# Optimization experiments

Measured on AMD Instinct MI355X. Metric: run time of the kernel, lower is better.

The kernel has to match this reference:

```python
import jax, jax.numpy as jnp
import numpy as np

N, E, G = 65536, 524288, 2048
HID, NLVL = 256, 50
SIG_BEGIN, SIG_END = 10.0, 0.01


def _silu(v):
    return v * jax.nn.sigmoid(v)


def _seg_sum(v, seg, num):
    return jax.ops.segment_sum(v, seg, num_segments=num)


def _seg_mean(v, seg, num):
    s = _seg_sum(v, seg, num)
    cnt = _seg_sum(jnp.ones((v.shape[0], 1), v.dtype), seg, num)
    return s / jnp.maximum(cnt, 1.0)


def setup_inputs() -> dict:
    key = jax.random.key(0)
    ks = jax.random.split(key, 24)
    sc = 1.0 / np.sqrt(HID)
    inp = {
        "x": jax.random.normal(ks[0], (N, HID), jnp.float32),
        "pos": jax.random.normal(ks[1], (N, 3), jnp.float32),
        "noise": jax.random.normal(ks[2], (N, 3), jnp.float32),
        "node2graph": jnp.sort(jax.random.randint(ks[3], (N,), 0, G)),
        "edge_index": jax.random.randint(ks[4], (2, E), 0, N),
        "noise_level": jax.random.randint(ks[5], (G,), 0, NLVL),
        # stand-in rep_model weights
        "W_node": jax.random.normal(ks[6], (HID, HID), jnp.float32) * sc,
        "W_msg": jax.random.normal(ks[7], (HID, HID), jnp.float32) * sc,
        "w_gate": jax.random.normal(ks[8], (HID, 1), jnp.float32) * sc,
        # node_dec
        "Wd1": jax.random.normal(ks[9], (HID, HID), jnp.float32) * sc,
        "bd1": jnp.zeros((HID,), jnp.float32),
        "Wd2": jax.random.normal(ks[10], (HID, HID), jnp.float32) * sc,
        "bd2": jnp.zeros((HID,), jnp.float32),
        # graph_dec
        "Wg1": jax.random.normal(ks[11], (HID, HID), jnp.float32) * sc,
        "bg1": jnp.zeros((HID,), jnp.float32),
        "Wg2": jax.random.normal(ks[12], (HID, 1), jnp.float32) * sc,
        "bg2": jnp.zeros((1,), jnp.float32),
        # noise_pred
        "Wp1": jax.random.normal(ks[13], (2 * HID, HID), jnp.float32) * sc,
        "bp1": jnp.zeros((HID,), jnp.float32),
        "Wp2": jax.random.normal(ks[14], (HID, NLVL), jnp.float32) * sc,
        "bp2": jnp.zeros((NLVL,), jnp.float32),
    }
    return inp


def _rep_model(x, pos, edge_index, W_node, W_msg, w_gate):
    # minimal one-layer equivariant stand-in for the external GNN rep_model
    row, col = edge_index[0], edge_index[1]
    msg = x[row] @ W_msg                                   # [E,H]
    agg = _seg_sum(msg, col, x.shape[0])                   # [N,H]
    xl = _silu(x @ W_node + agg)
    coef = _silu(msg @ w_gate)                             # [E,1]
    posl = pos + _seg_sum((pos[row] - pos[col]) * coef, col, x.shape[0])
    return xl, posl


def _fit_pos(pos_p, pos, n2g, num_g):
    # Kabsch alignment with batched 3x3 SVD (torch.svd: H = U S V^T, R = V U^T)
    center = _seg_mean(pos, n2g, num_g)                    # [G,3]
    pcenter = _seg_mean(pos_p, n2g, num_g)
    pos_c = pos - center[n2g]
    ppc = pos_p - pcenter[n2g]
    # H[g,i,j] = sum_n ppc[n,i]*pos_c[n,j] (matches repeat/repeat_interleave layout)
    Hmat = _seg_sum(jnp.einsum("ni,nj->nij", ppc, pos_c).reshape(-1, 9), n2g, num_g).reshape(-1, 3, 3)
    U, S, Vh = jnp.linalg.svd(Hmat)
    V = jnp.swapaxes(Vh, -1, -2)
    R = V @ jnp.swapaxes(U, -1, -2)                        # [G,3,3]
    t = center - jnp.einsum("gij,gj->gi", R, pcenter)
    return jnp.einsum("nij,nj->ni", R[n2g], pos_p) + t[n2g]


def reference(x, pos, noise, node2graph, edge_index, noise_level,
              W_node, W_msg, w_gate, Wd1, bd1, Wd2, bd2,
              Wg1, bg1, Wg2, bg2, Wp1, bp1, Wp2, bp2):
    num_g = noise_level.shape[0]
    sigmas = jnp.exp(jnp.linspace(np.log(SIG_BEGIN), np.log(SIG_END), NLVL)).astype(x.dtype)
    used_sigmas = sigmas[noise_level][node2graph][:, None]  # [N,1]

    # perturb (kabsch) + target, both no_grad in the original
    pos_p = jax.lax.stop_gradient(_fit_pos(pos + noise * used_sigmas, pos, node2graph, num_g))
    target = jax.lax.stop_gradient((pos - pos_p) / used_sigmas)

    def energy_rep(pin):
        xl, posl = _rep_model(x, pin, edge_index, W_node, W_msg, w_gate)
        xl = _silu(xl @ Wd1 + bd1) @ Wd2 + bd2             # node_dec
        xg = _seg_sum(xl, node2graph, num_g)               # scatter_add -> graph rep
        e = (_silu(xg @ Wg1 + bg1) @ Wg2 + bg2)[:, 0]      # graph_dec
        return e, xg, posl

    _, xg_noise, pred_pos = energy_rep(pos_p)
    pred_noise = (pred_pos - pos_p) / used_sigmas          # pred_mode == 'force'
    loss_den = _seg_sum(jnp.sum((pred_noise - target) ** 2, axis=-1), node2graph, num_g)

    _, xg_ori, _ = energy_rep(pos)
    graph_rep = jnp.concatenate([xg_ori, xg_noise], axis=1)
    logits = _silu(graph_rep @ Wp1 + bp1) @ Wp2 + bp2      # [G,NLVL]
    ce = jax.scipy.special.logsumexp(logits, axis=-1) - jnp.take_along_axis(
        logits, noise_level[:, None], axis=1)[:, 0]
    return jnp.stack([loss_den.mean(), ce.mean()])
```

## Files before the change

### kernel.cpp

```cpp
#include <hip/hip_runtime.h>
#include <math.h>

#define NN 65536
#define NE 524288
#define NG 2048
#define HD 256
#define NL 50

typedef unsigned short u16;
typedef unsigned char u8;
typedef __attribute__((ext_vector_type(8))) short short8;
typedef __attribute__((ext_vector_type(4))) float f32x4;
typedef __attribute__((ext_vector_type(4))) unsigned short us4;

__device__ __forceinline__ float bf2f(u16 h){
  union{unsigned int u; float f;} v; v.u = ((unsigned int)h)<<16; return v.f;
}
__device__ __forceinline__ u16 f2bf(float f){
  union{float f; unsigned int u;} v; v.f=f;
  return (u16)((v.u + 0x7FFFu + ((v.u>>16)&1u))>>16);
}
__device__ __forceinline__ float silu_f(float v){ return v/(1.0f+__expf(-v)); }
__device__ __forceinline__ u8 f2e4m3(float v){
  return (u8)__builtin_amdgcn_cvt_pk_fp8_f32(v, v, 0, false);
}
__device__ __forceinline__ float4 e4m3x4(unsigned w){
  float4 r;
  r.x = __builtin_amdgcn_cvt_f32_fp8(w, 0);
  r.y = __builtin_amdgcn_cvt_f32_fp8(w, 1);
  r.z = __builtin_amdgcn_cvt_f32_fp8(w, 2);
  r.w = __builtin_amdgcn_cvt_f32_fp8(w, 3);
  return r;
}

#define WRED(v) { v += __shfl_xor(v,1); v += __shfl_xor(v,2); v += __shfl_xor(v,4); \
                  v += __shfl_xor(v,8); v += __shfl_xor(v,16); v += __shfl_xor(v,32); }

__global__ void k_wmg(const float* __restrict__ Wm, const float* __restrict__ wgate,
                      float* __restrict__ wmg){
  int k = threadIdx.x;
  float s=0.f;
  for(int j=0;j<256;j++) s += Wm[k*256+j]*wgate[j];
  wmg[k]=s;
}

__global__ void k_front(const int* __restrict__ n2g,
                        const float* __restrict__ x, const int* __restrict__ ei,
                        const float* __restrict__ Wn, const float* __restrict__ Wm,
                        const float* __restrict__ Wd1, const float* __restrict__ Wd2,
                        const float* __restrict__ Wp1, const float* __restrict__ Wp2,
                        int* __restrict__ gstart,
                        u8* __restrict__ wn8, u8* __restrict__ wm8, u8* __restrict__ wd18,
                        u16* __restrict__ wd2b, u16* __restrict__ wpeb,
                        u16* __restrict__ wp2b, const float* __restrict__ wmg,
                        u8* __restrict__ xb8, float* __restrict__ cf,
                        int* __restrict__ cnt_e){
  int b = blockIdx.x, t = threadIdx.x;
  if(b < 257){
    int i = b*256 + t;
    if(i>NN) return;
    int cur  = (i<NN)? n2g[i] : NG;
    int prev = (i==0)? -1 : n2g[i-1];
    for(int g=prev+1; g<=cur; ++g) gstart[g]=i;
  } else if(b < 1601){
    int bb = b - 257;
    if(bb < 768){
      int m = bb>>8;
      int idx = (bb&255)*256 + t;
      int k = idx>>8, n = idx&255;
      const float* W = (m==0)? Wn : (m==1)? Wm : Wd1;
      u8* O = (m==0)? wn8 : (m==1)? wm8 : wd18;
      unsigned a = (unsigned)(n*256+k);
      O[a ^ ((unsigned)(n&15)<<3)] = f2e4m3(W[k*256+n]);
    } else if(bb < 1024){
      int idx = (bb-768)*256 + t; int k=idx>>8, n=idx&255;
      wd2b[n*256+k] = f2bf(Wd2[k*256+n]);
    } else if(bb < 1280){
      int idx = (bb-1024)*256 + t; int k=idx>>8, n=idx&255;
      wpeb[n*256+k] = f2bf(Wp1[k*256+n] + Wp1[(k+256)*256+n]);
    } else {
      int idx = (bb-1280)*256 + t; int k=idx&255, n=idx>>8;
      wp2b[n*256+k] = (n<NL)? f2bf(Wp2[k*NL+n]) : (u16)0;
    }
  } else if(b < 17985){
    int wave = t>>6, lane = t&63;
    int i = (b-1601)*4 + wave;
    float4 a = ((const float4*)(x + (size_t)i*256))[lane];
    float4 bb = ((const float4*)wmg)[lane];
    float s = a.x*bb.x + a.y*bb.y + a.z*bb.z + a.w*bb.w;
    unsigned w = __builtin_amdgcn_cvt_pk_fp8_f32(a.x, a.y, 0, false);
    w = __builtin_amdgcn_cvt_pk_fp8_f32(a.z, a.w, w, true);
    *(unsigned*)(xb8 + (size_t)i*256 + lane*4) = w;
    #pragma unroll
    for(int o=32;o;o>>=1) s += __shfl_down(s,o);
    if(lane==0) cf[i]=silu_f(s);
  } else {
    int e = (b-17985)*256 + t;
    if(e<NE) atomicAdd(&cnt_e[ei[NE+e]],1);
  }
}

__global__ __launch_bounds__(256) void k_mid(const float* __restrict__ pos,
        const float* __restrict__ noise, const int* __restrict__ gstart,
        const int* __restrict__ nl, float* __restrict__ sigg,
        float* __restrict__ posp, float* __restrict__ target,
        const int* __restrict__ cnt_e, int* __restrict__ start,
        int* __restrict__ bsum){
  int b = blockIdx.x, t = threadIdx.x;
  if(b >= 512){
    __shared__ int sh[256];
    int bb = b-512, i = bb*256+t;
    int v = cnt_e[i]; sh[t]=v; __syncthreads();
    #pragma unroll
    for(int o=1;o<256;o<<=1){
      int u = (t>=o)? sh[t-o]:0; __syncthreads(); sh[t]+=u; __syncthreads();
    }
    start[i] = sh[t]-v;
    if(t==255) bsum[bb]=sh[255];
    return;
  }
  int wid = (b<<2) + (t>>6);
  int lane = t & 63;
  int s0 = gstart[wid], s1 = gstart[wid+1];
  const double L0 =  2.3025850929940456840;
  const double L1 = -4.6051701859880913680;
  float sg = (float)exp(L0 + (double)nl[wid]*(L1-L0)/49.0);
  if(lane==0) sigg[wid]=sg;

  float sx=0,sy=0,sz=0, tx=0,ty=0,tz=0;
  for(int i=s0+lane;i<s1;i+=64){
    float px=pos[3*i],py=pos[3*i+1],pz=pos[3*i+2];
    sx+=px; sy+=py; sz+=pz;
    tx+=px+noise[3*i]*sg; ty+=py+noise[3*i+1]*sg; tz+=pz+noise[3*i+2]*sg;
  }
  WRED(sx); WRED(sy); WRED(sz); WRED(tx); WRED(ty); WRED(tz);
  float invc = 1.f/fmaxf((float)(s1-s0),1.f);
  float cx=sx*invc, cy=sy*invc, cz=sz*invc;
  float pcx=tx*invc, pcy=ty*invc, pcz=tz*invc;

  float h00=0,h01=0,h02=0,h10=0,h11=0,h12=0,h20=0,h21=0,h22=0;
  for(int i=s0+lane;i<s1;i+=64){
    float px=pos[3*i],py=pos[3*i+1],pz=pos[3*i+2];
    float a0=px+noise[3*i]*sg-pcx, a1=py+noise[3*i+1]*sg-pcy, a2=pz+noise[3*i+2]*sg-pcz;
    float b0=px-cx, b1=py-cy, b2=pz-cz;
    h00+=a0*b0; h01+=a0*b1; h02+=a0*b2;
    h10+=a1*b0; h11+=a1*b1; h12+=a1*b2;
    h20+=a2*b0; h21+=a2*b1; h22+=a2*b2;
  }
  WRED(h00); WRED(h01); WRED(h02); WRED(h10); WRED(h11); WRED(h12);
  WRED(h20); WRED(h21); WRED(h22);

  float X[3][3] = {{h00,h10,h20},{h01,h11,h21},{h02,h12,h22}};
  float nf=0.f;
  #pragma unroll
  for(int r=0;r<3;r++) for(int c=0;c<3;c++) nf += X[r][c]*X[r][c];
  nf = sqrtf(nf);
  if(nf < 1e-20f){
    #pragma unroll
    for(int r=0;r<3;r++) for(int c=0;c<3;c++) X[r][c]=(r==c)?1.f:0.f;
  } else {
    float s0f=1.f/nf;
    #pragma unroll
    for(int r=0;r<3;r++) for(int c=0;c<3;c++) X[r][c]*=s0f;
    for(int it=0; it<30; ++it){
      float a=X[0][0],bq=X[0][1],c=X[0][2];
      float d=X[1][0],e=X[1][1],f=X[1][2];
      float gg=X[2][0],h=X[2][1],ii=X[2][2];
      float A_= e*ii-f*h, B_=-(d*ii-f*gg), C_= d*h-e*gg;
      float D_=-(bq*ii-c*h), E_= a*ii-c*gg, F_=-(a*h-bq*gg);
      float G_= bq*f-c*e,  H_=-(a*f-c*d),  I_= a*e-bq*d;
      float det = a*A_ + bq*B_ + c*C_;
      if(!(fabsf(det) > 1e-25f)){
        if(it==0){
          for(int r=0;r<3;r++) for(int cc=0;cc<3;cc++) X[r][cc]=(r==cc)?1.f:0.f;
        }
        break;
      }
      float si = 0.5f/det;
      float Y00=0.5f*a + si*A_, Y01=0.5f*bq + si*B_, Y02=0.5f*c + si*C_;
      float Y10=0.5f*d + si*D_, Y11=0.5f*e + si*E_, Y12=0.5f*f + si*F_;
      float Y20=0.5f*gg+ si*G_, Y21=0.5f*h + si*H_, Y22=0.5f*ii+ si*I_;
      X[0][0]=Y00; X[0][1]=Y01; X[0][2]=Y02;
      X[1][0]=Y10; X[1][1]=Y11; X[1][2]=Y12;
      X[2][0]=Y20; X[2][1]=Y21; X[2][2]=Y22;
    }
  }
  float T0 = cx - (X[0][0]*pcx + X[0][1]*pcy + X[0][2]*pcz);
  float T1 = cy - (X[1][0]*pcx + X[1][1]*pcy + X[1][2]*pcz);
  float T2 = cz - (X[2][0]*pcx + X[2][1]*pcy + X[2][2]*pcz);
  float is = 1.f/sg;
  for(int i=s0+lane;i<s1;i+=64){
    float px=pos[3*i],py=pos[3*i+1],pz=pos[3*i+2];
    float qx=px+noise[3*i]*sg, qy=py+noise[3*i+1]*sg, qz=pz+noise[3*i+2]*sg;
    float ox = X[0][0]*qx + X[0][1]*qy + X[0][2]*qz + T0;
    float oy = X[1][0]*qx + X[1][1]*qy + X[1][2]*qz + T1;
    float oz = X[2][0]*qx + X[2][1]*qy + X[2][2]*qz + T2;
    posp[3*i]=ox; posp[3*i+1]=oy; posp[3*i+2]=oz;
    target[3*i]=(px-ox)*is; target[3*i+1]=(py-oy)*is; target[3*i+2]=(pz-oz)*is;
  }
}

__global__ void k_scan_b(int* __restrict__ bsum){
  __shared__ int sh[256];
  int t=threadIdx.x; int v=bsum[t]; sh[t]=v; __syncthreads();
  #pragma unroll
  for(int o=1;o<256;o<<=1){
    int u=(t>=o)?sh[t-o]:0; __syncthreads(); sh[t]+=u; __syncthreads();
  }
  bsum[t]=sh[t]-v;
}
__global__ void k_scan_c(int* __restrict__ start, const int* __restrict__ bsum,
                         int* __restrict__ cursor){
  int b=blockIdx.x, i=b*256+threadIdx.x;
  int v = start[i]+bsum[b];
  start[i]=v; cursor[i]=v;
  if(i==0) start[NN]=NE;
}
__global__ void k_scatter(const int* __restrict__ ei, int* __restrict__ cursor,
                          int* __restrict__ elist){
  int e = blockIdx.x*256+threadIdx.x; if(e>=NE) return;
  int c = ei[NE+e];
  int p = atomicAdd(&cursor[c],1);
  elist[p] = ei[e];
}

__global__ void k_gather8(const u8* __restrict__ xb8, const int* __restrict__ start,
                          const int* __restrict__ elist, u8* __restrict__ xs8){
  int lane = threadIdx.x & 63;
  int c = blockIdx.x*4 + (threadIdx.x>>6);
  int s0=start[c], s1=start[c+1];
  float a0=0.f,a1=0.f,a2=0.f,a3=0.f;
  int e=s0;
  for(; e+3<s1; e+=4){
    int r0=elist[e], r1=elist[e+1], r2=elist[e+2], r3=elist[e+3];
    unsigned w0 = *(const unsigned*)(xb8 + (size_t)r0*256 + lane*4);
    unsigned w1 = *(const unsigned*)(xb8 + (size_t)r1*256 + lane*4);
    unsigned w2 = *(const unsigned*)(xb8 + (size_t)r2*256 + lane*4);
    unsigned w3 = *(const unsigned*)(xb8 + (size_t)r3*256 + lane*4);
    float4 v0 = e4m3x4(w0), v1 = e4m3x4(w1), v2 = e4m3x4(w2), v3 = e4m3x4(w3);
    a0 += (v0.x+v1.x)+(v2.x+v3.x); a1 += (v0.y+v1.y)+(v2.y+v3.y);
    a2 += (v0.z+v1.z)+(v2.z+v3.z); a3 += (v0.w+v1.w)+(v2.w+v3.w);
  }
  for(; e<s1; ++e){
    unsigned w0 = *(const unsigned*)(xb8 + (size_t)elist[e]*256 + lane*4);
    float4 v0 = e4m3x4(w0);
    a0+=v0.x; a1+=v0.y; a2+=v0.z; a3+=v0.w;
  }
  unsigned w = __builtin_amdgcn_cvt_pk_fp8_f32(a0, a1, 0, false);
  w = __builtin_amdgcn_cvt_pk_fp8_f32(a2, a3, w, true);
  *(unsigned*)(xs8 + (size_t)c*256 + lane*4) = w;
}

__global__ __launch_bounds__(512) void gemmF8(
    const u8* __restrict__ A1, const u8* __restrict__ A2,
    const u8* __restrict__ Wn, const u8* __restrict__ Wm,
    const u8* __restrict__ Wd, const float* __restrict__ bd1,
    u8* __restrict__ outb){
  __shared__ u8 Bs[32768];
  __shared__ u8 XL[32768];
  int t = threadIdx.x;
  int wave = t>>6, lane = t&63;
  int lr = lane&15, lkgrp = lane>>4, lk8 = lkgrp*8;
  int m0 = blockIdx.x*128 + wave*16;
  char* xlw = (char*)XL + wave*4096;

  auto stage = [&](const u8* src){
    #pragma unroll
    for(int it=0; it<4; ++it){
      unsigned byte = (unsigned)(it*512 + t)*16;
      short8 v = *(const short8*)(src + byte);
      *(short8*)((char*)Bs + byte) = v;
    }
  };

  f32x4 acc[16];
  #pragma unroll
  for(int i=0;i<16;i++) acc[i]=(f32x4){0.f,0.f,0.f,0.f};

  for(int h=0; h<2; ++h){
    for(int m=0; m<2; ++m){
      __syncthreads();
      stage((m==0? Wn : Wm) + (size_t)h*32768);
      __syncthreads();
      const u8* Ab = (m==0? A1 : A2) + (size_t)(m0+lr)*256;
      #pragma unroll
      for(int k0=0;k0<256;k0+=32){
        long bx = *(const long*)(Ab + k0 + lk8);
        #pragma unroll
        for(int nt=0;nt<8;++nt){
          unsigned row = nt*16+lr;
          unsigned byte = (row<<8) + k0 + lk8;
          byte ^= ((row&15u)<<3);
          long a = *(const long*)((const char*)Bs + byte);
          acc[h*8+nt] = __builtin_amdgcn_mfma_f32_16x16x32_fp8_fp8(a,bx,acc[h*8+nt],0,0,0);
        }
      }
    }
  }

  #pragma unroll
  for(int h=0;h<2;++h){
    #pragma unroll
    for(int nt=0;nt<8;++nt){
      f32x4 v = acc[h*8+nt];
      unsigned pk = __builtin_amdgcn_cvt_pk_fp8_f32(silu_f(v[0]), silu_f(v[1]), 0, false);
      pk = __builtin_amdgcn_cvt_pk_fp8_f32(silu_f(v[2]), silu_f(v[3]), pk, true);
      unsigned byte = ((unsigned)lr<<8) + h*128 + nt*16 + lkgrp*4;
      byte ^= ((lr&15u)<<3);
      *(unsigned*)(xlw + byte) = pk;
    }
  }

  #pragma unroll
  for(int i=0;i<16;i++) acc[i]=(f32x4){0.f,0.f,0.f,0.f};
  for(int h=0;h<2;++h){
    __syncthreads();
    stage(Wd + (size_t)h*32768);
    __syncthreads();
    #pragma unroll
    for(int k0=0;k0<256;k0+=32){
      unsigned ab = ((unsigned)lr<<8) + k0 + lk8;
      ab ^= ((lr&15u)<<3);
      long bx = *(const long*)(xlw + ab);
      #pragma unroll
      for(int nt=0;nt<8;++nt){
        unsigned row = nt*16+lr;
        unsigned byte = (row<<8) + k0 + lk8;
        byte ^= ((row&15u)<<3);
        long a = *(const long*)((const char*)Bs + byte);
        acc[h*8+nt] = __builtin_amdgcn_mfma_f32_16x16x32_fp8_fp8(a,bx,acc[h*8+nt],0,0,0);
      }
    }
  }

  __syncthreads();
  #pragma unroll
  for(int h=0;h<2;++h){
    #pragma unroll
    for(int nt=0;nt<8;++nt){
      f32x4 v = acc[h*8+nt];
      int F = h*128 + nt*16 + lkgrp*4;
      unsigned pk = __builtin_amdgcn_cvt_pk_fp8_f32(silu_f(v[0]+bd1[F+0]), silu_f(v[1]+bd1[F+1]), 0, false);
      pk = __builtin_amdgcn_cvt_pk_fp8_f32(silu_f(v[2]+bd1[F+2]), silu_f(v[3]+bd1[F+3]), pk, true);
      unsigned row = (unsigned)(wave*16 + lr);
      unsigned byte = (row<<8) + (unsigned)F;
      byte ^= ((row&15u)<<3);
      *(unsigned*)((char*)Bs + byte) = pk;
    }
  }
  __syncthreads();
  #pragma unroll
  for(int it=0; it<8; ++it){
    unsigned byte = (unsigned)(it*512 + t)*8;
    unsigned src = byte ^ (((byte>>8)&15u)<<3);
    long v = *(const long*)((const char*)Bs + src);
    *(long*)(outb + (size_t)blockIdx.x*32768 + byte) = v;
  }
}

__global__ void k_tail(const int* __restrict__ start, const int* __restrict__ elist,
                       const float* __restrict__ posp, const float* __restrict__ cf,
                       const float* __restrict__ target, const float* __restrict__ sigg,
                       const int* __restrict__ n2g, float* __restrict__ accum,
                       const u8* __restrict__ h18, const int* __restrict__ gstart,
                       u16* __restrict__ sgb){
  int b = blockIdx.x, t = threadIdx.x;
  if(b < 256){
    int i = b*256+t;
    float s=0.f;
    {
      int s0=start[i], s1=start[i+1];
      float px=posp[i*3+0], py=posp[i*3+1], pz=posp[i*3+2];
      float dx=0.f, dy=0.f, dz=0.f;
      for(int e=s0;e<s1;e++){
        int r=elist[e];
        float c=cf[r];
        dx += (posp[r*3+0]-px)*c;
        dy += (posp[r*3+1]-py)*c;
        dz += (posp[r*3+2]-pz)*c;
      }
      float is = 1.f/sigg[n2g[i]];
      float d0 = dx*is - target[i*3+0];
      float d1 = dy*is - target[i*3+1];
      float d2 = dz*is - target[i*3+2];
      s = d0*d0+d1*d1+d2*d2;
    }
    #pragma unroll
    for(int o=32;o;o>>=1) s += __shfl_down(s,o);
    if((t&63)==0) atomicAdd(&accum[0], s);
  } else {
    int lane = t&63;
    int g = (b-256)*4 + (t>>6);
    int s0=gstart[g], s1=gstart[g+1];
    float a0=0.f,a1=0.f,a2=0.f,a3=0.f;
    for(int i=s0;i<s1;i++){
      unsigned w = *(const unsigned*)(h18 + (size_t)i*256 + lane*4);
      float4 v = e4m3x4(w);
      a0+=v.x; a1+=v.y; a2+=v.z; a3+=v.w;
    }
    us4 o; o.x=f2bf(a0); o.y=f2bf(a1); o.z=f2bf(a2); o.w=f2bf(a3);
    *(us4*)(sgb + (size_t)g*256 + lane*4) = o;
  }
}

__global__ __launch_bounds__(256) void k_head3(const u16* __restrict__ sgb,
        const int* __restrict__ gstart, const float* __restrict__ bd2,
        const u16* __restrict__ wd2b, const u16* __restrict__ wpeb,
        const float* __restrict__ bp1, const u16* __restrict__ wp2b,
        const float* __restrict__ bp2, const int* __restrict__ nlv,
        float* __restrict__ accum){
  __shared__ u16 S[64*256];
  int t = threadIdx.x;
  int wave = t>>6, lane = t&63;
  int lr = lane&15, lkgrp = lane>>4, lk = lkgrp*8;
  int g0 = blockIdx.x*64;
  int rw = wave*16;

  f32x4 acc[16];
  #pragma unroll
  for(int nt=0;nt<16;nt++) acc[nt]=(f32x4){0.f,0.f,0.f,0.f};
  #pragma unroll
  for(int k0=0;k0<256;k0+=32){
    short8 a = *(const short8*)(sgb + (size_t)(g0+rw+lr)*256 + k0 + lk);
    #pragma unroll
    for(int nt=0;nt<16;nt++){
      short8 b = *(const short8*)(wd2b + (size_t)(nt*16+lr)*256 + k0 + lk);
      acc[nt] = __builtin_amdgcn_mfma_f32_16x16x32_bf16(a,b,acc[nt],0,0,0);
    }
  }
  #pragma unroll
  for(int j=0;j<4;j++){
    unsigned gl = rw + lkgrp*4 + j;
    float cnt = (float)(gstart[g0+gl+1]-gstart[g0+gl]);
    #pragma unroll
    for(int nt=0;nt<16;nt++){
      int c = nt*16+lr;
      float v = acc[nt][j] + cnt*bd2[c];
      *(u16*)((char*)S + ((((gl<<9) + c*2)) ^ ((gl&7u)<<4))) = f2bf(v);
    }
  }

  #pragma unroll
  for(int nt=0;nt<16;nt++) acc[nt]=(f32x4){0.f,0.f,0.f,0.f};
  #pragma unroll
  for(int k0=0;k0<256;k0+=32){
    unsigned row = rw+lr;
    short8 a = *(const short8*)((char*)S + (((row<<9) + (k0+lk)*2) ^ ((row&7u)<<4)));
    #pragma unroll
    for(int nt=0;nt<16;nt++){
      short8 b = *(const short8*)(wpeb + (size_t)(nt*16+lr)*256 + k0 + lk);
      acc[nt] = __builtin_amdgcn_mfma_f32_16x16x32_bf16(a,b,acc[nt],0,0,0);
    }
  }
  #pragma unroll
  for(int j=0;j<4;j++){
    unsigned gl = rw + lkgrp*4 + j;
    #pragma unroll
    for(int nt=0;nt<16;nt++){
      int c = nt*16+lr;
      float v = silu_f(acc[nt][j] + bp1[c]);
      *(u16*)((char*)S + ((((gl<<9) + c*2)) ^ ((gl&7u)<<4))) = f2bf(v);
    }
  }

  #pragma unroll
  for(int nt=0;nt<4;nt++) acc[nt]=(f32x4){0.f,0.f,0.f,0.f};
  #pragma unroll
  for(int k0=0;k0<256;k0+=32){
    unsigned row = rw+lr;
    short8 a = *(const short8*)((char*)S + (((row<<9) + (k0+lk)*2) ^ ((row&7u)<<4)));
    #pragma unroll
    for(int nt=0;nt<4;nt++){
      short8 b = *(const short8*)(wp2b + (size_t)(nt*16+lr)*256 + k0 + lk);
      acc[nt] = __builtin_amdgcn_mfma_f32_16x16x32_bf16(a,b,acc[nt],0,0,0);
    }
  }
  float bp[4];
  #pragma unroll
  for(int nt=0;nt<4;nt++){
    int c = nt*16+lr;
    bp[nt] = (c<NL)? bp2[c] : 0.f;
  }
  float s = 0.f;
  #pragma unroll
  for(int j=0;j<4;j++){
    int g = g0 + rw + lkgrp*4 + j;
    int tgt = nlv[g];
    float mx = -1e30f, pk = 0.f;
    float lg[4];
    #pragma unroll
    for(int nt=0;nt<4;nt++){
      int c = nt*16+lr;
      lg[nt] = (c<NL)? (acc[nt][j] + bp[nt]) : -1e30f;
      mx = fmaxf(mx, lg[nt]);
      if(c==tgt) pk = lg[nt];
    }
    #pragma unroll
    for(int o=1;o<16;o<<=1) mx = fmaxf(mx, __shfl_xor(mx,o));
    float se = 0.f;
    #pragma unroll
    for(int nt=0;nt<4;nt++) se += __expf(lg[nt]-mx);
    #pragma unroll
    for(int o=1;o<16;o<<=1) se += __shfl_xor(se,o);
    #pragma unroll
    for(int o=1;o<16;o<<=1) pk += __shfl_xor(pk,o);
    s += logf(se)+mx - pk;
  }
  if(lr==0) atomicAdd(&accum[1], s);
}

__global__ void k_final(const float* __restrict__ accum, float* __restrict__ out){
  out[0] = accum[0]/(float)NG;
  out[1] = accum[1]/(float)NG;
}

extern "C" void kernel_launch(void* const* d_in, const int* in_sizes, int n_in,
                              void* d_out, int out_size, void* d_ws, size_t ws_size,
                              hipStream_t stream){
  (void)in_sizes; (void)n_in; (void)out_size; (void)ws_size;
  const float* x      = (const float*)d_in[0];
  const float* pos    = (const float*)d_in[1];
  const float* noise  = (const float*)d_in[2];
  const int*   n2g    = (const int*)d_in[3];
  const int*   ei     = (const int*)d_in[4];
  const int*   nl     = (const int*)d_in[5];
  const float* W_node = (const float*)d_in[6];
  const float* W_msg  = (const float*)d_in[7];
  const float* w_gate = (const float*)d_in[8];
  const float* Wd1    = (const float*)d_in[9];
  const float* bd1    = (const float*)d_in[10];
  const float* Wd2    = (const float*)d_in[11];
  const float* bd2    = (const float*)d_in[12];
  const float* Wp1    = (const float*)d_in[17];
  const float* bp1    = (const float*)d_in[18];
  const float* Wp2    = (const float*)d_in[19];
  const float* bp2    = (const float*)d_in[20];
  float* out = (float*)d_out;

  char* w = (char*)d_ws;
  size_t off = 0;
  auto alloc = [&](size_t bytes)->void*{
    void* p = w + off;
    off += (bytes + 255) & ~(size_t)255;
    return p;
  };

  size_t zstart = off;
  int*   cnt_e   = (int*)alloc((size_t)NN*4);
  float* accum   = (float*)alloc(2*4);
  size_t zend = off;

  u8*   xb8  = (u8*)alloc((size_t)NN*HD);
  u8*   xs8  = (u8*)alloc((size_t)NN*HD);
  u8*   h18  = (u8*)alloc((size_t)NN*HD);
  u16*  sgb  = (u16*)alloc((size_t)NG*HD*2);
  float* sigg   = (float*)alloc((size_t)NG*4);
  float* posp   = (float*)alloc((size_t)NN*3*4);
  float* target = (float*)alloc((size_t)NN*3*4);
  float* cf     = (float*)alloc((size_t)NN*4);
  int*  gstart  = (int*)alloc((size_t)(NG+1)*4);
  int*  start   = (int*)alloc((size_t)(NN+1)*4);
  int*  cursor  = (int*)alloc((size_t)NN*4);
  int*  bsum    = (int*)alloc((size_t)256*4);
  int*  elist   = (int*)alloc((size_t)NE*4);
  u8*   wn8     = (u8*)alloc((size_t)HD*HD);
  u8*   wm8     = (u8*)alloc((size_t)HD*HD);
  u8*   wd18    = (u8*)alloc((size_t)HD*HD);
  u16*  wd2b    = (u16*)alloc((size_t)HD*HD*2);
  u16*  wpeb    = (u16*)alloc((size_t)HD*HD*2);
  u16*  wp2b    = (u16*)alloc((size_t)64*HD*2);
  float* wmg    = (float*)alloc((size_t)HD*4);

  (void)hipMemsetAsync(w+zstart, 0, zend-zstart, stream);

  k_wmg  <<<1,256,0,stream>>>(W_msg,w_gate,wmg);

  k_front<<<20033,256,0,stream>>>(n2g,x,ei,W_node,W_msg,Wd1,Wd2,Wp1,Wp2,
                                  gstart,wn8,wm8,wd18,wd2b,wpeb,wp2b,wmg,
                                  xb8,cf,cnt_e);
  k_mid  <<<768,256,0,stream>>>(pos,noise,gstart,nl,sigg,posp,target,
                                cnt_e,start,bsum);
  k_scan_b<<<1,256,0,stream>>>(bsum);
  k_scan_c<<<NN/256,256,0,stream>>>(start,bsum,cursor);
  k_scatter<<<NE/256,256,0,stream>>>(ei,cursor,elist);

  k_gather8<<<NN/4,256,0,stream>>>(xb8,start,elist,xs8);
  gemmF8   <<<512,512,0,stream>>>(xb8,xs8,wn8,wm8,wd18,bd1,h18);

  k_tail <<<768,256,0,stream>>>(start,elist,posp,cf,target,sigg,n2g,accum,
                                h18,gstart,sgb);
  k_head3<<<NG/64,256,0,stream>>>(sgb,gstart,bd2,wd2b,wpeb,bp1,wp2b,bp2,nl,accum);
  k_final<<<1,1,0,stream>>>(accum,out);
}
```

Baseline: 251.0 us.

## Restructure fp8 GEMM to 4 waves each computing two 16-row tiles per half

```diff
diff --git a/kernel.cpp b/kernel.cpp
--- a/kernel.cpp
+++ b/kernel.cpp
@@ -251,7 +251,7 @@
   *(unsigned*)(xs8 + (size_t)c*256 + lane*4) = w;
 }
 
-__global__ __launch_bounds__(512) void gemmF8(
+__global__ __launch_bounds__(256) void gemmF8(
     const u8* __restrict__ A1, const u8* __restrict__ A2,
     const u8* __restrict__ Wn, const u8* __restrict__ Wm,
     const u8* __restrict__ Wd, const float* __restrict__ bd1,
@@ -261,100 +261,106 @@
   int t = threadIdx.x;
   int wave = t>>6, lane = t&63;
   int lr = lane&15, lkgrp = lane>>4, lk8 = lkgrp*8;
-  int m0 = blockIdx.x*128 + wave*16;
-  char* xlw = (char*)XL + wave*4096;
+  int m0b = blockIdx.x*128;
+  int nw0 = wave*32;
 
   auto stage = [&](const u8* src){
     #pragma unroll
-    for(int it=0; it<4; ++it){
-      unsigned byte = (unsigned)(it*512 + t)*16;
+    for(int it=0; it<8; ++it){
+      unsigned byte = (unsigned)(it*256 + t)*16;
       short8 v = *(const short8*)(src + byte);
       *(short8*)((char*)Bs + byte) = v;
     }
   };
 
-  f32x4 acc[16];
-  #pragma unroll
-  for(int i=0;i<16;i++) acc[i]=(f32x4){0.f,0.f,0.f,0.f};
+  f32x4 acc[2][8];
 
   for(int h=0; h<2; ++h){
     for(int m=0; m<2; ++m){
       __syncthreads();
       stage((m==0? Wn : Wm) + (size_t)h*32768);
       __syncthreads();
-      const u8* Ab = (m==0? A1 : A2) + (size_t)(m0+lr)*256;
+      if(m==0){
+        #pragma unroll
+        for(int mi=0;mi<2;mi++)
+          #pragma unroll
+          for(int nt=0;nt<8;nt++) acc[mi][nt]=(f32x4){0.f,0.f,0.f,0.f};
+      }
+      const u8* Ab = (m==0? A1 : A2);
       #pragma unroll
       for(int k0=0;k0<256;k0+=32){
-        long bx = *(const long*)(Ab + k0 + lk8);
+        long bx0 = *(const long*)(Ab + (size_t)(m0b+nw0   +lr)*256 + k0 + lk8);
+        long bx1 = *(const long*)(Ab + (size_t)(m0b+nw0+16+lr)*256 + k0 + lk8);
         #pragma unroll
         for(int nt=0;nt<8;++nt){
           unsigned row = nt*16+lr;
-          unsigned byte = (row<<8) + k0 + lk8;
-          byte ^= ((row&15u)<<3);
+          unsigned byte = ((row<<8) + k0 + lk8) ^ ((row&15u)<<3);
           long a = *(const long*)((const char*)Bs + byte);
-          acc[h*8+nt] = __builtin_amdgcn_mfma_f32_16x16x32_fp8_fp8(a,bx,acc[h*8+nt],0,0,0);
+          acc[0][nt] = __builtin_amdgcn_mfma_f32_16x16x32_fp8_fp8(a,bx0,acc[0][nt],0,0,0);
+          acc[1][nt] = __builtin_amdgcn_mfma_f32_16x16x32_fp8_fp8(a,bx1,acc[1][nt],0,0,0);
         }
       }
     }
-  }
-
-  #pragma unroll
-  for(int h=0;h<2;++h){
-    #pragma unroll
-    for(int nt=0;nt<8;++nt){
-      f32x4 v = acc[h*8+nt];
-      unsigned pk = __builtin_amdgcn_cvt_pk_fp8_f32(silu_f(v[0]), silu_f(v[1]), 0, false);
-      pk = __builtin_amdgcn_cvt_pk_fp8_f32(silu_f(v[2]), silu_f(v[3]), pk, true);
-      unsigned byte = ((unsigned)lr<<8) + h*128 + nt*16 + lkgrp*4;
-      byte ^= ((lr&15u)<<3);
-      *(unsigned*)(xlw + byte) = pk;
-    }
-  }
-
-  #pragma unroll
-  for(int i=0;i<16;i++) acc[i]=(f32x4){0.f,0.f,0.f,0.f};
+    #pragma unroll
+    for(int mi=0;mi<2;++mi){
+      unsigned node = (unsigned)(nw0 + mi*16 + lr);
+      #pragma unroll
+      for(int nt=0;nt<8;++nt){
+        f32x4 v = acc[mi][nt];
+        unsigned pk = __builtin_amdgcn_cvt_pk_fp8_f32(silu_f(v[0]), silu_f(v[1]), 0, false);
+        pk = __builtin_amdgcn_cvt_pk_fp8_f32(silu_f(v[2]), silu_f(v[3]), pk, true);
+        unsigned byte = ((node<<8) + h*128 + nt*16 + lkgrp*4) ^ ((node&15u)<<3);
+        *(unsigned*)(XL + byte) = pk;
+      }
+    }
+  }
+
   for(int h=0;h<2;++h){
     __syncthreads();
     stage(Wd + (size_t)h*32768);
     __syncthreads();
     #pragma unroll
+    for(int mi=0;mi<2;mi++)
+      #pragma unroll
+      for(int nt=0;nt<8;nt++) acc[mi][nt]=(f32x4){0.f,0.f,0.f,0.f};
+    #pragma unroll
     for(int k0=0;k0<256;k0+=32){
-      unsigned ab = ((unsigned)lr<<8) + k0 + lk8;
-      ab ^= ((lr&15u)<<3);
-      long bx = *(const long*)(xlw + ab);
+      unsigned r0 = nw0+lr, r1 = nw0+16+lr;
+      long bx0 = *(const long*)(XL + (((r0<<8) + k0 + lk8) ^ ((r0&15u)<<3)));
+      long bx1 = *(const long*)(XL + (((r1<<8) + k0 + lk8) ^ ((r1&15u)<<3)));
       #pragma unroll
       for(int nt=0;nt<8;++nt){
         unsigned row = nt*16+lr;
-        unsigned byte = (row<<8) + k0 + lk8;
-        byte ^= ((row&15u)<<3);
+        unsigned byte = ((row<<8) + k0 + lk8) ^ ((row&15u)<<3);
         long a = *(const long*)((const char*)Bs + byte);
-        acc[h*8+nt] = __builtin_amdgcn_mfma_f32_16x16x32_fp8_fp8(a,bx,acc[h*8+nt],0,0,0);
+        acc[0][nt] = __builtin_amdgcn_mfma_f32_16x16x32_fp8_fp8(a,bx0,acc[0][nt],0,0,0);
+        acc[1][nt] = __builtin_amdgcn_mfma_f32_16x16x32_fp8_fp8(a,bx1,acc[1][nt],0,0,0);
       }
     }
-  }
-
-  __syncthreads();
-  #pragma unroll
-  for(int h=0;h<2;++h){
-    #pragma unroll
-    for(int nt=0;nt<8;++nt){
-      f32x4 v = acc[h*8+nt];
-      int F = h*128 + nt*16 + lkgrp*4;
-      unsigned pk = __builtin_amdgcn_cvt_pk_fp8_f32(silu_f(v[0]+bd1[F+0]), silu_f(v[1]+bd1[F+1]), 0, false);
-      pk = __builtin_amdgcn_cvt_pk_fp8_f32(silu_f(v[2]+bd1[F+2]), silu_f(v[3]+bd1[F+3]), pk, true);
-      unsigned row = (unsigned)(wave*16 + lr);
-      unsigned byte = (row<<8) + (unsigned)F;
-      byte ^= ((row&15u)<<3);
-      *(unsigned*)((char*)Bs + byte) = pk;
-    }
-  }
-  __syncthreads();
-  #pragma unroll
-  for(int it=0; it<8; ++it){
-    unsigned byte = (unsigned)(it*512 + t)*8;
-    unsigned src = byte ^ (((byte>>8)&15u)<<3);
-    long v = *(const long*)((const char*)Bs + src);
-    *(long*)(outb + (size_t)blockIdx.x*32768 + byte) = v;
+    __syncthreads();
+    #pragma unroll
+    for(int mi=0;mi<2;++mi){
+      unsigned node = (unsigned)(nw0 + mi*16 + lr);
+      #pragma unroll
+      for(int nt=0;nt<8;++nt){
+        f32x4 v = acc[mi][nt];
+        int F = h*128 + nt*16 + lkgrp*4;
+        unsigned pk = __builtin_amdgcn_cvt_pk_fp8_f32(silu_f(v[0]+bd1[F+0]), silu_f(v[1]+bd1[F+1]), 0, false);
+        pk = __builtin_amdgcn_cvt_pk_fp8_f32(silu_f(v[2]+bd1[F+2]), silu_f(v[3]+bd1[F+3]), pk, true);
+        unsigned Floc = (unsigned)(nt*16 + lkgrp*4);
+        unsigned byte = ((node<<7) + Floc) ^ ((node&15u)<<3);
+        *(unsigned*)((char*)Bs + byte) = pk;
+      }
+    }
+    __syncthreads();
+    #pragma unroll
+    for(int it=0; it<8; ++it){
+      unsigned y = (unsigned)(it*256 + t)*8;
+      unsigned src = y ^ (((y>>7)&15u)<<3);
+      long v = *(const long*)((const char*)Bs + src);
+      size_t gaddr = (size_t)(m0b + (y>>7))*256 + h*128 + (y&127u);
+      *(long*)(outb + gaddr) = v;
+    }
   }
 }
 
@@ -585,7 +591,7 @@
   k_scatter<<<NE/256,256,0,stream>>>(ei,cursor,elist);
 
   k_gather8<<<NN/4,256,0,stream>>>(xb8,start,elist,xs8);
-  gemmF8   <<<512,512,0,stream>>>(xb8,xs8,wn8,wm8,wd18,bd1,h18);
+  gemmF8   <<<512,256,0,stream>>>(xb8,xs8,wn8,wm8,wd18,bd1,h18);
 
   k_tail <<<768,256,0,stream>>>(start,elist,posp,cf,target,sigg,n2g,accum,
                                 h18,gstart,sgb);
```

After: 280.7 us. 11.8% more time.

## Double-buffer weight staging in fused FP8 GEMM and fold block scan into scan_c

Applied to the files above, without the earlier changes.

```diff
diff --git a/kernel.cpp b/kernel.cpp
--- a/kernel.cpp
+++ b/kernel.cpp
@@ -200,19 +200,18 @@
   }
 }
 
-__global__ void k_scan_b(int* __restrict__ bsum){
+__global__ void k_scan_c(int* __restrict__ start, const int* __restrict__ bsum,
+                         int* __restrict__ cursor){
   __shared__ int sh[256];
-  int t=threadIdx.x; int v=bsum[t]; sh[t]=v; __syncthreads();
+  int b=blockIdx.x, t=threadIdx.x;
+  sh[t]=bsum[t]; __syncthreads();
   #pragma unroll
   for(int o=1;o<256;o<<=1){
     int u=(t>=o)?sh[t-o]:0; __syncthreads(); sh[t]+=u; __syncthreads();
   }
-  bsum[t]=sh[t]-v;
-}
-__global__ void k_scan_c(int* __restrict__ start, const int* __restrict__ bsum,
-                         int* __restrict__ cursor){
-  int b=blockIdx.x, i=b*256+threadIdx.x;
-  int v = start[i]+bsum[b];
+  int base = (b==0)? 0 : sh[b-1];
+  int i = b*256+t;
+  int v = start[i] + base;
   start[i]=v; cursor[i]=v;
   if(i==0) start[NN]=NE;
 }
@@ -263,73 +262,87 @@
   int lr = lane&15, lkgrp = lane>>4, lk8 = lkgrp*8;
   int m0 = blockIdx.x*128 + wave*16;
   char* xlw = (char*)XL + wave*4096;
-
-  auto stage = [&](const u8* src){
-    #pragma unroll
-    for(int it=0; it<4; ++it){
-      unsigned byte = (unsigned)(it*512 + t)*16;
-      short8 v = *(const short8*)(src + byte);
-      *(short8*)((char*)Bs + byte) = v;
-    }
+  int row_t = t>>2, col_t = (t&3)*32;
+
+  f32x4 acc[16];
+  #pragma unroll
+  for(int i=0;i<16;i++) acc[i]=(f32x4){0.f,0.f,0.f,0.f};
+
+  short8 pre0, pre1;
+  auto preload = [&](int u){
+    const u8* W = (u>=8)? Wd : (((u>>1)&1)? Wm : Wn);
+    int h  = (u>=8)? ((u>>1)&1) : (u>>2);
+    int kh = u&1;
+    const u8* s = W + (size_t)(h*128 + row_t)*256 + kh*128 + col_t;
+    pre0 = *(const short8*)(s);
+    pre1 = *(const short8*)(s+16);
   };
-
-  f32x4 acc[16];
-  #pragma unroll
-  for(int i=0;i<16;i++) acc[i]=(f32x4){0.f,0.f,0.f,0.f};
-
-  for(int h=0; h<2; ++h){
-    for(int m=0; m<2; ++m){
-      __syncthreads();
-      stage((m==0? Wn : Wm) + (size_t)h*32768);
-      __syncthreads();
+  auto commit = [&](int p){
+    char* d = (char*)Bs + p*16384 + row_t*128 + col_t;
+    *(short8*)(d)    = pre0;
+    *(short8*)(d+16) = pre1;
+  };
+
+  preload(0); commit(0);
+  #pragma unroll
+  for(int u=0; u<12; ++u){
+    if(u<11) preload(u+1);
+    __syncthreads();
+    const char* buf = (const char*)Bs + (u&1)*16384;
+    int kh = u&1;
+    int hsel = (u>=8)? ((u>>1)&1) : (u>>2);
+    if(u<8){
+      int m = (u>>1)&1;
       const u8* Ab = (m==0? A1 : A2) + (size_t)(m0+lr)*256;
       #pragma unroll
-      for(int k0=0;k0<256;k0+=32){
+      for(int kq=0;kq<4;++kq){
+        int k0 = kh*128 + kq*32;
         long bx = *(const long*)(Ab + k0 + lk8);
         #pragma unroll
         for(int nt=0;nt<8;++nt){
           unsigned row = nt*16+lr;
-          unsigned byte = (row<<8) + k0 + lk8;
-          byte ^= ((row&15u)<<3);
-          long a = *(const long*)((const char*)Bs + byte);
-          acc[h*8+nt] = __builtin_amdgcn_mfma_f32_16x16x32_fp8_fp8(a,bx,acc[h*8+nt],0,0,0);
+          unsigned byte = (row*128u + kq*32 + lk8) ^ ((row&15u)<<3);
+          long a = *(const long*)(buf + byte);
+          acc[hsel*8+nt] = __builtin_amdgcn_mfma_f32_16x16x32_fp8_fp8(a,bx,acc[hsel*8+nt],0,0,0);
         }
       }
-    }
-  }
-
-  #pragma unroll
-  for(int h=0;h<2;++h){
-    #pragma unroll
-    for(int nt=0;nt<8;++nt){
-      f32x4 v = acc[h*8+nt];
-      unsigned pk = __builtin_amdgcn_cvt_pk_fp8_f32(silu_f(v[0]), silu_f(v[1]), 0, false);
-      pk = __builtin_amdgcn_cvt_pk_fp8_f32(silu_f(v[2]), silu_f(v[3]), pk, true);
-      unsigned byte = ((unsigned)lr<<8) + h*128 + nt*16 + lkgrp*4;
-      byte ^= ((lr&15u)<<3);
-      *(unsigned*)(xlw + byte) = pk;
-    }
-  }
-
-  #pragma unroll
-  for(int i=0;i<16;i++) acc[i]=(f32x4){0.f,0.f,0.f,0.f};
-  for(int h=0;h<2;++h){
-    __syncthreads();
-    stage(Wd + (size_t)h*32768);
-    __syncthreads();
-    #pragma unroll
-    for(int k0=0;k0<256;k0+=32){
-      unsigned ab = ((unsigned)lr<<8) + k0 + lk8;
-      ab ^= ((lr&15u)<<3);
-      long bx = *(const long*)(xlw + ab);
+    } else {
+      #pragma unroll
+      for(int kq=0;kq<4;++kq){
+        int k0 = kh*128 + kq*32;
+        unsigned ab = (((unsigned)lr<<8) + k0 + lk8) ^ ((lr&15u)<<3);
+        long bx = *(const long*)(xlw + ab);
+        #pragma unroll
+        for(int nt=0;nt<8;++nt){
+          unsigned row = nt*16+lr;
+          unsigned byte = (row*128u + kq*32 + lk8) ^ ((row&15u)<<3);
+          long a = *(const long*)(buf + byte);
+          acc[hsel*8+nt] = __builtin_amdgcn_mfma_f32_16x16x32_fp8_fp8(a,bx,acc[hsel*8+nt],0,0,0);
+        }
+      }
+    }
+    if(u<11) commit((u&1)^1);
+    if(u==3){
       #pragma unroll
       for(int nt=0;nt<8;++nt){
-        unsigned row = nt*16+lr;
-        unsigned byte = (row<<8) + k0 + lk8;
-        byte ^= ((row&15u)<<3);
-        long a = *(const long*)((const char*)Bs + byte);
-        acc[h*8+nt] = __builtin_amdgcn_mfma_f32_16x16x32_fp8_fp8(a,bx,acc[h*8+nt],0,0,0);
+        f32x4 v = acc[nt];
+        unsigned pk = __builtin_amdgcn_cvt_pk_fp8_f32(silu_f(v[0]), silu_f(v[1]), 0, false);
+        pk = __builtin_amdgcn_cvt_pk_fp8_f32(silu_f(v[2]), silu_f(v[3]), pk, true);
+        unsigned byte = (((unsigned)lr<<8) + nt*16 + lkgrp*4) ^ ((lr&15u)<<3);
+        *(unsigned*)(xlw + byte) = pk;
       }
+    }
+    if(u==7){
+      #pragma unroll
+      for(int nt=0;nt<8;++nt){
+        f32x4 v = acc[8+nt];
+        unsigned pk = __builtin_amdgcn_cvt_pk_fp8_f32(silu_f(v[0]), silu_f(v[1]), 0, false);
+        pk = __builtin_amdgcn_cvt_pk_fp8_f32(silu_f(v[2]), silu_f(v[3]), pk, true);
+        unsigned byte = (((unsigned)lr<<8) + 128 + nt*16 + lkgrp*4) ^ ((lr&15u)<<3);
+        *(unsigned*)(xlw + byte) = pk;
+      }
+      #pragma unroll
+      for(int i=0;i<16;i++) acc[i]=(f32x4){0.f,0.f,0.f,0.f};
     }
   }
 
@@ -343,8 +356,7 @@
       unsigned pk = __builtin_amdgcn_cvt_pk_fp8_f32(silu_f(v[0]+bd1[F+0]), silu_f(v[1]+bd1[F+1]), 0, false);
       pk = __builtin_amdgcn_cvt_pk_fp8_f32(silu_f(v[2]+bd1[F+2]), silu_f(v[3]+bd1[F+3]), pk, true);
       unsigned row = (unsigned)(wave*16 + lr);
-      unsigned byte = (row<<8) + (unsigned)F;
-      byte ^= ((row&15u)<<3);
+      unsigned byte = ((row<<8) + (unsigned)F) ^ ((row&15u)<<3);
       *(unsigned*)((char*)Bs + byte) = pk;
     }
   }
@@ -580,7 +592,6 @@
                                   xb8,cf,cnt_e);
   k_mid  <<<768,256,0,stream>>>(pos,noise,gstart,nl,sigg,posp,target,
                                 cnt_e,start,bsum);
-  k_scan_b<<<1,256,0,stream>>>(bsum);
   k_scan_c<<<NN/256,256,0,stream>>>(start,bsum,cursor);
   k_scatter<<<NE/256,256,0,stream>>>(ei,cursor,elist);
 
```

New measurement: 237.9 us. 1.06x faster.
